# Kernel tuning notes

Hardware: AMD Instinct MI355X
Metric: run time of the kernel (lower is better)

The kernel has to match this reference:

```python
import jax, jax.numpy as jnp
import numpy as np

N_E = 8192
E_DIM = 256
BETA = 0.25
ORTHO_COEF = 1.0


def setup_inputs() -> dict:
    key = jax.random.key(0)
    k1, k2 = jax.random.split(key)
    z = jax.random.normal(k1, (16, E_DIM, 32, 32), dtype=jnp.float32)
    # nn.Embedding init: uniform(-1/n_e, 1/n_e)
    codebook = jax.random.uniform(k2, (N_E, E_DIM), dtype=jnp.float32,
                                  minval=-1.0 / N_E, maxval=1.0 / N_E)
    return {"z": z, "codebook": codebook}


def reference(z, codebook):
    B, C, H, W = z.shape
    n_e = codebook.shape[0]
    zt = jnp.transpose(z, (0, 2, 3, 1))            # (B,H,W,C)
    zf = zt.reshape(-1, C)                          # (N,C)

    # L2 distances: ||z||^2 + ||e||^2 - 2 z.e
    d = (jnp.sum(zf * zf, axis=1, keepdims=True)
         + jnp.sum(codebook * codebook, axis=1)
         - 2.0 * jnp.matmul(zf, codebook.T))        # (N, n_e)
    idx = jnp.argmin(d, axis=1)                     # (N,)

    z_q_flat = codebook[idx]                        # gather == one-hot @ codebook
    z_q = z_q_flat.reshape(zt.shape)                # (B,H,W,C)

    sg = jax.lax.stop_gradient
    loss = (BETA * jnp.mean((sg(z_q) - zt) ** 2)
            + jnp.mean((z_q - sg(zt)) ** 2))

    # ortho regularizer (force_emb_len_1 == False branch)
    wn = codebook / jnp.linalg.norm(codebook, axis=1, keepdims=True)
    diff = jnp.matmul(wn, wn.T) - jnp.eye(n_e, dtype=codebook.dtype)
    ortho_reg_term = ORTHO_COEF * jnp.sum(diff ** 2) / (n_e ** 2)

    # straight-through estimator
    z_q_st = zt + sg(z_q - zt)

    # perplexity from mean one-hot usage
    N = zf.shape[0]
    counts = jnp.zeros((n_e,), dtype=zt.dtype).at[idx].add(1.0)
    e_mean = counts / N
    perplexity = jnp.exp(-jnp.sum(e_mean * jnp.log(e_mean + 1e-10)))

    z_q_out = jnp.transpose(z_q_st, (0, 3, 1, 2))   # (B,C,H,W)
    return z_q_out, loss, ortho_reg_term, perplexity, idx
```

## Files before the change

### kernel.cpp

```cpp
#include <hip/hip_runtime.h>
#include <hip/hip_bf16.h>
#include <math.h>


#define N_E     8192
#define C_DIM   256
#define N_VEC   16384
#define N_ELEM  4194304
#define MARGIN  6.0e-4f

#define WS_COUNTS   0
#define WS_M        32768
#define WS_ACCUM    294912
#define WS_LISTLEN  294944
#define WS_CE       295200
#define WS_RN       327968
#define WS_A        360736
#define WS_KEYS     426272
#define WS_LISTS    557344
#define WS_TILEMIN  4751648
#define WS_ZBF      8945952
#define WS_CBBF     17334560
#define WS_ZT       21528864

typedef short short8v __attribute__((ext_vector_type(8)));
typedef float f32x4  __attribute__((ext_vector_type(4)));

__device__ inline unsigned short f2bf(float f) {
    unsigned int x = __float_as_uint(f);
    return (unsigned short)((x + 0x7fffu + ((x >> 16) & 1u)) >> 16);
}

__device__ inline void gload16(const void* g, void* l) {
    __builtin_amdgcn_global_load_lds(
        (const __attribute__((address_space(1))) unsigned int*)g,
        (__attribute__((address_space(3))) unsigned int*)l, 16, 0, 0);
}

__global__ __launch_bounds__(256) void k_prep(const float* __restrict__ cb,
                                              const float* __restrict__ z,
                                              float* __restrict__ ce,
                                              float* __restrict__ rn,
                                              unsigned short* __restrict__ cbbf,
                                              unsigned short* __restrict__ zbf,
                                              float* __restrict__ zT,
                                              float* __restrict__ A,
                                              float* __restrict__ M,
                                              int* __restrict__ counts,
                                              int* __restrict__ listlen,
                                              double* __restrict__ accum) {
    __shared__ float tile[64 * 260];
    const int tid = threadIdx.x;

    if (blockIdx.x < 8192) {
        const int j = blockIdx.x;
        if (tid == 0) {
            counts[j] = 0;
            if (j < 64) listlen[j] = 0;
            if (j == 0) {
                accum[0] = 0.0; accum[1] = 0.0; accum[2] = 0.0; accum[3] = 0.0;
            }
        }
        float v = cb[(size_t)j * C_DIM + tid];
        cbbf[(size_t)j * C_DIM + tid] = f2bf(v);
        float s = v * v;
        #pragma unroll
        for (int off = 32; off > 0; off >>= 1) s += __shfl_down(s, off, 64);
        if ((tid & 63) == 0) tile[tid >> 6] = s;
        __syncthreads();
        if (tid == 0) {
            float t = tile[0] + tile[1] + tile[2] + tile[3];
            ce[j] = t;
            rn[j] = 1.0f / sqrtf(t);
        }
    } else {
        const int bz = blockIdx.x - 8192;
        M[bz * 256 + tid] = 0.0f;

        const int n0 = bz * 64;
        const int b = n0 >> 10, hw0 = n0 & 1023;
        const float* zp = z + (size_t)b * 262144 + hw0;

        const int hw = tid & 63, cg = tid >> 6;
        #pragma unroll 8
        for (int p = 0; p < 64; ++p) {
            int c = p * 4 + cg;
            tile[hw * 260 + c] = zp[(size_t)c * 1024 + hw];
        }
        __syncthreads();

        if (tid < 64) {
            float a = 0.0f;
            #pragma unroll 8
            for (int c = 0; c < C_DIM; ++c) {
                float v = tile[tid * 260 + c];
                a = fmaf(v, v, a);
            }
            A[n0 + tid] = a;
        }

        const int r = tid >> 2, q = tid & 3;
        unsigned short* dst = zbf + (size_t)(n0 + r) * C_DIM + q * 64;
        float* dstT         = zT  + (size_t)(n0 + r) * C_DIM + q * 64;
        const float* src = &tile[r * 260 + q * 64];
        #pragma unroll
        for (int i = 0; i < 8; ++i) {
            f32x4 lo = *(const f32x4*)&src[i * 8];
            f32x4 hi = *(const f32x4*)&src[i * 8 + 4];
            *(f32x4*)&dstT[i * 8]     = lo;
            *(f32x4*)&dstT[i * 8 + 4] = hi;
            short8v u;
            #pragma unroll
            for (int x = 0; x < 4; ++x) { u[x] = (short)f2bf(lo[x]); u[4 + x] = (short)f2bf(hi[x]); }
            *(short8v*)(dst + i * 8) = u;
        }
    }
}

__global__ __launch_bounds__(256) void k_mfma(const unsigned short* __restrict__ zbf,
                                              const unsigned short* __restrict__ cbbf,
                                              float* __restrict__ tilemin) {
    __shared__ unsigned short As[128 * 64];
    __shared__ unsigned short Bs[128 * 64];
    __shared__ float smin[128][2];

    const int tid = threadIdx.x;
    const int lin = blockIdx.x;
    const int x = lin & 7, r = lin >> 3;
    const int jp = r >> 7, q = r & 127;
    const int by = x * 16 + (q >> 3), bx = jp * 8 + (q & 7);
    const int n0 = by * 128, j0 = bx * 128;
    const int wave = tid >> 6, lane = tid & 63;
    const int wx = wave & 1, wy = wave >> 1;
    const int g = lane >> 4, c = lane & 15;

    const int lrow  = lane >> 3;
    const int lslot = (lane & 7) ^ lrow;
    const int rbase = wave * 32;

    f32x4 acc[4][4];
    #pragma unroll
    for (int i = 0; i < 4; ++i)
        #pragma unroll
        for (int j = 0; j < 4; ++j) acc[i][j] = (f32x4){0.f, 0.f, 0.f, 0.f};

    for (int kc = 0; kc < C_DIM; kc += 64) {
        __syncthreads();
        #pragma unroll
        for (int i = 0; i < 4; ++i) {
            const int row8 = rbase + i * 8;
            const unsigned short* ga =
                zbf  + (size_t)(n0 + row8 + lrow) * C_DIM + kc + lslot * 8;
            const unsigned short* gb =
                cbbf + (size_t)(j0 + row8 + lrow) * C_DIM + kc + lslot * 8;
            gload16(ga, &As[row8 * 64]);
            gload16(gb, &Bs[row8 * 64]);
        }
        __syncthreads();

        #pragma unroll
        for (int kk = 0; kk < 2; ++kk) {
            short8v a[4], b[4];
            #pragma unroll
            for (int f = 0; f < 4; ++f) {
                const int row = wy * 64 + f * 16 + c;
                a[f] = *(const short8v*)&As[row * 64 + (((kk * 4 + g) ^ (c & 7)) * 8)];
            }
            #pragma unroll
            for (int f = 0; f < 4; ++f) {
                const int row = wx * 64 + f * 16 + c;
                b[f] = *(const short8v*)&Bs[row * 64 + (((kk * 4 + g) ^ (c & 7)) * 8)];
            }
            #pragma unroll
            for (int nf = 0; nf < 4; ++nf)
                #pragma unroll
                for (int jf = 0; jf < 4; ++jf)
                    acc[nf][jf] = __builtin_amdgcn_mfma_f32_16x16x32_bf16(
                        a[nf], b[jf], acc[nf][jf], 0, 0, 0);
        }
    }

    #pragma unroll
    for (int nf = 0; nf < 4; ++nf) {
        #pragma unroll
        for (int rr = 0; rr < 4; ++rr) {
            float mx = acc[nf][0][rr];
            #pragma unroll
            for (int jf = 1; jf < 4; ++jf) mx = fmaxf(mx, acc[nf][jf][rr]);
            #pragma unroll
            for (int off = 1; off < 16; off <<= 1)
                mx = fmaxf(mx, __shfl_xor(mx, off, 64));
            if (c == 0) smin[wy * 64 + nf * 16 + g * 4 + rr][wx] = -2.0f * mx;
        }
    }
    __syncthreads();
    if (tid < 128)
        tilemin[(size_t)bx * N_VEC + n0 + tid] = fminf(smin[tid][0], smin[tid][1]);
}

__global__ __launch_bounds__(256) void k_candgram(const float* __restrict__ tilemin,
                                                  unsigned long long* __restrict__ keys,
                                                  int* __restrict__ listlen,
                                                  int* __restrict__ lists,
                                                  const float* __restrict__ cb,
                                                  const float* __restrict__ rn,
                                                  float* __restrict__ M) {
    __shared__ float buf[2 * 64 * 68];
    const int tid = threadIdx.x;

    if (blockIdx.x < 256) {
        float* red   = buf;
        float* thr_s = buf + 256;
        const int nl = tid & 63, tg = tid >> 6;
        const int n = blockIdx.x * 64 + nl;

        float m = 3.4e38f;
        #pragma unroll
        for (int i = 0; i < 16; ++i)
            m = fminf(m, tilemin[(size_t)(tg * 16 + i) * N_VEC + n]);
        red[tg * 64 + nl] = m;
        __syncthreads();
        if (tg == 0) {
            thr_s[nl] = fminf(fminf(red[0 * 64 + nl], red[1 * 64 + nl]),
                              fminf(red[2 * 64 + nl], red[3 * 64 + nl])) + MARGIN;
            keys[n] = ~0ull;
        }
        __syncthreads();
        const float thr = thr_s[nl];

        #pragma unroll
        for (int i = 0; i < 16; ++i) {
            const int t = tg * 16 + i;
            bool qq = tilemin[(size_t)t * N_VEC + n] <= thr;
            unsigned long long mask = __ballot(qq);
            if (mask) {
                int ldr = __ffsll(mask) - 1;
                int base = 0;
                if (nl == ldr) base = atomicAdd(&listlen[t], __popcll(mask));
                base = __shfl(base, ldr, 64);
                if (qq) {
                    int pre = __popcll(mask & ((1ull << nl) - 1ull));
                    lists[t * N_VEC + base + pre] = n;
                }
            }
        }
    } else {
        float* aT = buf;
        float* bT = buf + 64 * 68;
        const int gidx = blockIdx.x - 256;
        const int k0 = (gidx & 3) * 64, l0 = ((gidx >> 2) & 3) * 64;
        const int jc0 = (gidx >> 4) * 256;
        const int tk = tid & 15, tl = tid >> 4;
        float acc[4][4];
        #pragma unroll
        for (int i = 0; i < 4; ++i)
            #pragma unroll
            for (int l = 0; l < 4; ++l) acc[i][l] = 0.0f;

        for (int jc = jc0; jc < jc0 + 256; jc += 64) {
            __syncthreads();
            {
                int kk = tid & 63, jj0 = tid >> 6;
                #pragma unroll
                for (int p = 0; p < 16; ++p) {
                    int jj = p * 4 + jj0;
                    float rr = rn[jc + jj];
                    const float* row = cb + (size_t)(jc + jj) * C_DIM;
                    aT[jj * 68 + kk] = row[k0 + kk] * rr;
                    bT[jj * 68 + kk] = row[l0 + kk] * rr;
                }
            }
            __syncthreads();
            #pragma unroll 8
            for (int jj = 0; jj < 64; ++jj) {
                float4 av = *(const float4*)&aT[jj * 68 + tk * 4];
                float4 bv = *(const float4*)&bT[jj * 68 + tl * 4];
                float a4[4] = {av.x, av.y, av.z, av.w};
                float b4[4] = {bv.x, bv.y, bv.z, bv.w};
                #pragma unroll
                for (int i = 0; i < 4; ++i)
                    #pragma unroll
                    for (int l = 0; l < 4; ++l)
                        acc[i][l] = fmaf(a4[i], b4[l], acc[i][l]);
            }
        }
        #pragma unroll
        for (int i = 0; i < 4; ++i)
            #pragma unroll
            for (int l = 0; l < 4; ++l)
                atomicAdd(&M[(size_t)(k0 + tk * 4 + i) * C_DIM + l0 + tl * 4 + l], acc[i][l]);
    }
}

__global__ __launch_bounds__(256) void k_refine2(const float* __restrict__ zT,
                                                 const float* __restrict__ cb,
                                                 const float* __restrict__ ce,
                                                 const float* __restrict__ A,
                                                 const int* __restrict__ listlen,
                                                 const int* __restrict__ lists,
                                                 unsigned long long* __restrict__ keys) {
    __shared__ float e_s[128 * 68];
    __shared__ float z_s[32 * 68];
    __shared__ int   rows_s[32];

    const int t = blockIdx.x;
    const int len = listlen[t];
    const int tid = threadIdx.x;
    const int jg = tid & 31, rg = tid >> 5;
    const int j0 = t * 128;

    for (int b0 = blockIdx.y * 32; b0 < len; b0 += 128 * 32) {
        const int nrows = min(32, len - b0);
        __syncthreads();
        if (tid < 32)
            rows_s[tid] = lists[t * N_VEC + b0 + min(tid, nrows - 1)];

        float acc[4][4];
        #pragma unroll
        for (int rr = 0; rr < 4; ++rr)
            #pragma unroll
            for (int jj = 0; jj < 4; ++jj) acc[rr][jj] = 0.0f;

        for (int kc = 0; kc < C_DIM; kc += 64) {
            __syncthreads();
            {
                int jr = tid >> 1, ko = (tid & 1) * 32;
                #pragma unroll
                for (int i = 0; i < 8; ++i)
                    *(float4*)&e_s[jr * 68 + ko + i * 4] =
                        *(const float4*)&cb[(size_t)(j0 + jr) * C_DIM + kc + ko + i * 4];
            }
            {
                int r = tid >> 3, ko = (tid & 7) * 8;
                const float* zp = &zT[(size_t)rows_s[r] * C_DIM + kc + ko];
                *(float4*)&z_s[r * 68 + ko]     = *(const float4*)&zp[0];
                *(float4*)&z_s[r * 68 + ko + 4] = *(const float4*)&zp[4];
            }
            __syncthreads();

            #pragma unroll
            for (int k4 = 0; k4 < 16; ++k4) {
                float4 ef[4], zf[4];
                #pragma unroll
                for (int jj = 0; jj < 4; ++jj)
                    ef[jj] = *(const float4*)&e_s[(jg + 32 * jj) * 68 + k4 * 4];
                #pragma unroll
                for (int rr = 0; rr < 4; ++rr)
                    zf[rr] = *(const float4*)&z_s[(rg * 4 + rr) * 68 + k4 * 4];
                #pragma unroll
                for (int kk = 0; kk < 4; ++kk)
                    #pragma unroll
                    for (int rr = 0; rr < 4; ++rr)
                        #pragma unroll
                        for (int jj = 0; jj < 4; ++jj)
                            acc[rr][jj] = fmaf(((const float*)&zf[rr])[kk],
                                               ((const float*)&ef[jj])[kk], acc[rr][jj]);
            }
        }

        #pragma unroll
        for (int rr = 0; rr < 4; ++rr) {
            const int n = rows_s[rg * 4 + rr];
            const float An = A[n];
            unsigned long long best = ~0ull;
            #pragma unroll
            for (int jj = 0; jj < 4; ++jj) {
                int j = j0 + jg + 32 * jj;
                float tt = An + ce[j];
                float d = fmaf(-2.0f, acc[rr][jj], tt);
                unsigned int sd = __float_as_uint(d);
                sd = (sd & 0x80000000u) ? ~sd : (sd | 0x80000000u);
                unsigned long long key = ((unsigned long long)sd << 32) | (unsigned)j;
                best = key < best ? key : best;
            }
            #pragma unroll
            for (int off = 16; off > 0; off >>= 1) {
                unsigned long long o = __shfl_xor(best, off, 64);
                best = o < best ? o : best;
            }
            if (jg == 0) atomicMin(&keys[n], best);
        }
    }
}

__global__ __launch_bounds__(256) void k_gather(const float* __restrict__ z,
                                                const float* __restrict__ cb,
                                                const unsigned long long* __restrict__ keys,
                                                const float* __restrict__ M,
                                                float* __restrict__ out,
                                                float* __restrict__ out_idx,
                                                int* __restrict__ counts,
                                                double* __restrict__ accum) {
    const int tid = threadIdx.x;
    __shared__ int sidx[32];
    __shared__ double sh[4];

    if (blockIdx.x >= 512) {
        const int bid = blockIdx.x - 512;
        float4 v = *(const float4*)&M[bid * 1024 + tid * 4];
        double s = (double)v.x * v.x + (double)v.y * v.y
                 + (double)v.z * v.z + (double)v.w * v.w;
        #pragma unroll
        for (int off = 32; off > 0; off >>= 1) s += __shfl_down(s, off, 64);
        if ((tid & 63) == 0) sh[tid >> 6] = s;
        __syncthreads();
        if (tid == 0) atomicAdd(&accum[1], sh[0] + sh[1] + sh[2] + sh[3]);
        return;
    }

    int bh = blockIdx.x;
    int b = bh >> 5, h = bh & 31;
    if (tid < 32) {
        int n = b * 1024 + h * 32 + tid;
        unsigned long long k = keys[n];
        int idx = (int)(k & 0xFFFFFFFFull);
        sidx[tid] = idx;
        out_idx[n] = (float)idx;
        atomicAdd(&counts[idx], 1);
    }
    __syncthreads();
    int w = tid & 31, cy = tid >> 5;
    int jid = sidx[w];
    const float* cbr = cb + (size_t)jid * C_DIM;
    size_t zb = (size_t)b * 262144 + h * 32 + w;

    double acc = 0.0;
    #pragma unroll 4
    for (int cc = 0; cc < 32; ++cc) {
        int c = cc * 8 + cy;
        float e = cbr[c];
        size_t zi = zb + (size_t)c * 1024;
        float d = e - z[zi];
        out[zi] = e;
        acc += (double)(d * d);
    }
    #pragma unroll
    for (int off = 32; off > 0; off >>= 1) acc += __shfl_down(acc, off, 64);
    if ((tid & 63) == 0) sh[tid >> 6] = acc;
    __syncthreads();
    if (tid == 0) atomicAdd(&accum[0], sh[0] + sh[1] + sh[2] + sh[3]);
}

__global__ __launch_bounds__(256) void k_final(const int* __restrict__ counts,
                                               const double* __restrict__ accum,
                                               float* __restrict__ out_scalars) {
    const int tid = threadIdx.x;
    __shared__ double sh[4];
    double h = 0.0;
    for (int j = tid; j < N_E; j += 256) {
        double p = counts[j] * (1.0 / (double)N_VEC);
        h += p * log(p + 1e-10);
    }
    #pragma unroll
    for (int off = 32; off > 0; off >>= 1) h += __shfl_down(h, off, 64);
    if ((tid & 63) == 0) sh[tid >> 6] = h;
    __syncthreads();
    if (tid == 0) {
        double H = sh[0] + sh[1] + sh[2] + sh[3];
        out_scalars[0] = (float)(1.25 * accum[0] / (double)N_ELEM);
        out_scalars[1] = (float)((accum[1] - (double)N_E) / ((double)N_E * N_E));
        out_scalars[2] = (float)exp(-H);
    }
}

extern "C" void kernel_launch(void* const* d_in, const int* in_sizes, int n_in,
                              void* d_out, int out_size, void* d_ws, size_t ws_size,
                              hipStream_t stream) {
    (void)in_sizes; (void)n_in; (void)out_size; (void)ws_size;
    const float* z  = (const float*)d_in[0];
    const float* cb = (const float*)d_in[1];
    float* out = (float*)d_out;

    char* ws = (char*)d_ws;
    int* counts            = (int*)(ws + WS_COUNTS);
    float* M               = (float*)(ws + WS_M);
    double* accum          = (double*)(ws + WS_ACCUM);
    int* listlen           = (int*)(ws + WS_LISTLEN);
    float* ce              = (float*)(ws + WS_CE);
    float* rn              = (float*)(ws + WS_RN);
    float* A               = (float*)(ws + WS_A);
    unsigned long long* keys = (unsigned long long*)(ws + WS_KEYS);
    int* lists             = (int*)(ws + WS_LISTS);
    float* tilemin         = (float*)(ws + WS_TILEMIN);
    unsigned short* zbf    = (unsigned short*)(ws + WS_ZBF);
    unsigned short* cbbf   = (unsigned short*)(ws + WS_CBBF);
    float* zT              = (float*)(ws + WS_ZT);

    float* out_scalars = out + N_ELEM;
    float* out_idx     = out + N_ELEM + 3;

    k_prep<<<8448, 256, 0, stream>>>(cb, z, ce, rn, cbbf, zbf, zT, A,
                                     M, counts, listlen, accum);
    k_mfma<<<8192, 256, 0, stream>>>(zbf, cbbf, tilemin);
    k_candgram<<<768, 256, 0, stream>>>(tilemin, keys, listlen, lists, cb, rn, M);
    k_refine2<<<dim3(64, 128), 256, 0, stream>>>(zT, cb, ce, A, listlen, lists, keys);
    k_gather<<<576, 256, 0, stream>>>(z, cb, keys, M, out, out_idx, counts, accum);
    k_final<<<1, 256, 0, stream>>>(counts, accum, out_scalars);
}
```

Baseline: 341.8 us.

## Double-buffer LDS tiles in MFMA distance kernel with async prefetch

The MFMA distance kernel now uses two LDS buffers per operand. It issues the first two K-chunk loads up front and prefetches chunk ci+2 right after computing chunk ci. Explicit vmcnt waits and raw s_barriers with sched_barrier fences replace the load/sync/compute sequence, so global-to-LDS traffic overlaps MFMA work. The cost is twice the LDS per block, which may lower occupancy, and correctness now depends on hand-counted outstanding loads.

```diff
diff --git a/kernel.cpp b/kernel.cpp
--- a/kernel.cpp
+++ b/kernel.cpp
@@ -117,11 +117,12 @@
     }
 }
 
+#define MF_BUF (128 * 64)
+
 __global__ __launch_bounds__(256) void k_mfma(const unsigned short* __restrict__ zbf,
                                               const unsigned short* __restrict__ cbbf,
                                               float* __restrict__ tilemin) {
-    __shared__ unsigned short As[128 * 64];
-    __shared__ unsigned short Bs[128 * 64];
+    __shared__ unsigned short SB[2][2][MF_BUF];
     __shared__ float smin[128][2];
 
     const int tid = threadIdx.x;
@@ -144,20 +145,29 @@
         #pragma unroll
         for (int j = 0; j < 4; ++j) acc[i][j] = (f32x4){0.f, 0.f, 0.f, 0.f};
 
-    for (int kc = 0; kc < C_DIM; kc += 64) {
-        __syncthreads();
+    #pragma unroll
+    for (int s = 0; s < 2; ++s) {
+        const int kc = s * 64;
         #pragma unroll
         for (int i = 0; i < 4; ++i) {
             const int row8 = rbase + i * 8;
-            const unsigned short* ga =
-                zbf  + (size_t)(n0 + row8 + lrow) * C_DIM + kc + lslot * 8;
-            const unsigned short* gb =
-                cbbf + (size_t)(j0 + row8 + lrow) * C_DIM + kc + lslot * 8;
-            gload16(ga, &As[row8 * 64]);
-            gload16(gb, &Bs[row8 * 64]);
-        }
-        __syncthreads();
-
+            gload16(zbf  + (size_t)(n0 + row8 + lrow) * C_DIM + kc + lslot * 8,
+                    &SB[s][0][row8 * 64]);
+            gload16(cbbf + (size_t)(j0 + row8 + lrow) * C_DIM + kc + lslot * 8,
+                    &SB[s][1][row8 * 64]);
+        }
+    }
+
+    #pragma unroll
+    for (int ci = 0; ci < 4; ++ci) {
+        if (ci < 3) asm volatile("s_waitcnt vmcnt(8)" ::: "memory");
+        else        asm volatile("s_waitcnt vmcnt(0)" ::: "memory");
+        __builtin_amdgcn_sched_barrier(0);
+        __builtin_amdgcn_s_barrier();
+        __builtin_amdgcn_sched_barrier(0);
+
+        const unsigned short* As = SB[ci & 1][0];
+        const unsigned short* Bs = SB[ci & 1][1];
         #pragma unroll
         for (int kk = 0; kk < 2; ++kk) {
             short8v a[4], b[4];
@@ -177,6 +187,21 @@
                 for (int jf = 0; jf < 4; ++jf)
                     acc[nf][jf] = __builtin_amdgcn_mfma_f32_16x16x32_bf16(
                         a[nf], b[jf], acc[nf][jf], 0, 0, 0);
+        }
+
+        __builtin_amdgcn_sched_barrier(0);
+        __builtin_amdgcn_s_barrier();
+        __builtin_amdgcn_sched_barrier(0);
+        if (ci < 2) {
+            const int kc = (ci + 2) * 64;
+            #pragma unroll
+            for (int i = 0; i < 4; ++i) {
+                const int row8 = rbase + i * 8;
+                gload16(zbf  + (size_t)(n0 + row8 + lrow) * C_DIM + kc + lslot * 8,
+                        &SB[ci & 1][0][row8 * 64]);
+                gload16(cbbf + (size_t)(j0 + row8 + lrow) * C_DIM + kc + lslot * 8,
+                        &SB[ci & 1][1][row8 * 64]);
+            }
         }
     }
 
```

New measurement: 365.6 us. 1.07x slower.
